# Optimization experiments

Hardware: AMD Instinct MI355X
Metric: run time of the kernel (lower is better)

The kernel has to match this reference:

```python
import jax, jax.numpy as jnp
import numpy as np

EPS = 1e-5
BOUNDARY = 1.0 - EPS
TEMP = 0.5  # temperature from init_kwargs


def _safe_sqrt(t):
    # sqrt with zero (not inf/nan) gradient at t<=0; matches the analytic clamp
    # in the original custom backward (clamp(z*beta, min=eps)).
    pos = t > 0
    return jnp.where(pos, jnp.sqrt(jnp.where(pos, t, 1.0)), 0.0)


def _poincare_sim(z):
    # z: [2N, D]. Pairwise Poincare distance computed via the matmul identity
    # ||u-v||^2 = ||u||^2 + ||v||^2 - 2 u.v instead of a (2N,2N,D) broadcast.
    raw = jnp.sum(z * z, axis=-1)                      # [2N] unclamped sq norms
    sqc = jnp.clip(raw, 0.0, BOUNDARY)                 # clamped as in forward
    sqdist = jnp.maximum(raw[:, None] + raw[None, :] - 2.0 * (z @ z.T), 0.0)
    x = sqdist / ((1.0 - sqc[:, None]) * (1.0 - sqc[None, :])) * 2.0 + 1.0
    dist = jnp.log(x + _safe_sqrt(x * x - 1.0))        # arcosh(x)
    return 1.0 / (1.0 + dist)                          # Poincare similarity


def setup_inputs() -> dict:
    key = jax.random.key(0)
    k1, k2, k3, k4 = jax.random.split(key, 4)
    N, D = 4096, 8

    def ball(kg, kr):
        g = jax.random.normal(kg, (N, D), dtype=jnp.float32)
        r = jax.random.uniform(kr, (N, 1), dtype=jnp.float32) * 0.85
        return g * r / (jnp.linalg.norm(g, axis=-1, keepdims=True) + 1e-6)

    return {"z_i": ball(k1, k2), "z_j": ball(k3, k4)}


def reference(z_i, z_j):
    N = z_i.shape[0]
    z = jnp.concatenate([z_i, z_j], axis=0)            # [2N, D]
    sim = _poincare_sim(z)                             # [2N, 2N]
    idx = jnp.arange(N)
    # diag(sim, +N) and diag(sim, -N): positive pairs
    positives = jnp.concatenate([sim[idx, idx + N], sim[idx + N, idx]])  # [2N]
    mask = 1.0 - jnp.eye(2 * N, dtype=sim.dtype)       # exclude self-similarity
    denom = jnp.sum(mask * jnp.exp(sim / TEMP), axis=1)  # [2N]
    all_losses = -(positives / TEMP - jnp.log(denom))
    return jnp.sum(all_losses) / (2 * N)
```

## Files before the change

### kernel.cpp

```cpp
#include <hip/hip_runtime.h>
#include <math.h>


#define D 8
#define QS 12
#define TWO_N 8192
#define HALF_N 4096
constexpr int BLOCK = 256;
constexpr int JC    = 32;
constexpr int NTILE = 2176;
constexpr int NSEG  = 368;
constexpr int SEG_LO = 1776;
#define BOUNDARY (1.0f - 1e-5f)
#define LN2 0.6931471805599453f

typedef float f32x2 __attribute__((ext_vector_type(2)));

__device__ __forceinline__ float frcp(float x)  { return __builtin_amdgcn_rcpf(x); }
__device__ __forceinline__ float fsqrt(float x) { return __builtin_amdgcn_sqrtf(x); }
__device__ __forceinline__ float flog2(float x) { return __builtin_amdgcn_logf(x); }
__device__ __forceinline__ f32x2 splat(float v) { return (f32x2){v, v}; }

__device__ __forceinline__ float dpp_wave_sum(float v) {
    int x;
    x = __builtin_amdgcn_update_dpp(0, __float_as_int(v), 0x111, 0xf, 0xf, false);
    v += __int_as_float(x);
    x = __builtin_amdgcn_update_dpp(0, __float_as_int(v), 0x112, 0xf, 0xf, false);
    v += __int_as_float(x);
    x = __builtin_amdgcn_update_dpp(0, __float_as_int(v), 0x114, 0xf, 0xe, false);
    v += __int_as_float(x);
    x = __builtin_amdgcn_update_dpp(0, __float_as_int(v), 0x118, 0xf, 0xc, false);
    v += __int_as_float(x);
    x = __builtin_amdgcn_update_dpp(0, __float_as_int(v), 0x142, 0xa, 0xf, false);
    v += __int_as_float(x);
    x = __builtin_amdgcn_update_dpp(0, __float_as_int(v), 0x143, 0xc, 0xf, false);
    v += __int_as_float(x);
    return v;
}

__global__ __launch_bounds__(256) void prep_kernel(
    const float* __restrict__ zi, const float* __restrict__ zj,
    float* __restrict__ q, float* __restrict__ denom, float* __restrict__ out,
    float2* __restrict__ tab)
{
    const int row = blockIdx.x * 256 + threadIdx.x;
    const float* src = (row < HALF_N) ? (zi + (size_t)row * D)
                                      : (zj + (size_t)(row - HALF_N) * D);
    float4 a = *(const float4*)(src);
    float4 b = *(const float4*)(src + 4);
    float raw = a.x*a.x + a.y*a.y + a.z*a.z + a.w*a.w
              + b.x*b.x + b.y*b.y + b.z*b.z + b.w*b.w;
    float inv = frcp(1.0f - fminf(raw, BOUNDARY));
    float* dst = q + (size_t)row * QS;
    *(float4*)(dst)     = a;
    *(float4*)(dst + 4) = b;
    *(float4*)(dst + 8) = make_float4(inv, inv * raw, 0.0f, 0.0f);
    denom[row] = 0.0f;
    if (row == 0) out[0] = 0.0f;

    if (row < NSEG) {
        const int m0 = row + SEG_LO;
        const int m1 = m0 + 1;
        float ua_f = __uint_as_float(((unsigned)(m0 >> 4) << 23) | ((unsigned)(m0 & 15) << 19));
        float ub_f = __uint_as_float(((unsigned)(m1 >> 4) << 23) | ((unsigned)(m1 & 15) << 19));
        double ua = (double)ua_f, ub = (double)ub_f;
        double ga = exp(2.0 / (1.0 + log(1.0 + ua + sqrt(ua * (ua + 2.0)))));
        double gb = exp(2.0 / (1.0 + log(1.0 + ub + sqrt(ub * (ub + 2.0)))));
        double sl = (gb - ga) / (ub - ua);
        double ic = ga - sl * ua;
        tab[row] = make_float2((float)sl, (float)ic);
    }
}

__device__ __forceinline__ f32x2 dot_col(const f32x2* __restrict__ p2,
                                         const float* __restrict__ qq)
{
    float4 a  = *(const float4*)(qq);
    float4 bb = *(const float4*)(qq + 4);
    float2 c  = *(const float2*)(qq + 8);
    f32x2 x = splat(0.0f);
    x = __builtin_elementwise_fma(p2[0], splat(a.x),  x);
    x = __builtin_elementwise_fma(p2[1], splat(a.y),  x);
    x = __builtin_elementwise_fma(p2[2], splat(a.z),  x);
    x = __builtin_elementwise_fma(p2[3], splat(a.w),  x);
    x = __builtin_elementwise_fma(p2[4], splat(bb.x), x);
    x = __builtin_elementwise_fma(p2[5], splat(bb.y), x);
    x = __builtin_elementwise_fma(p2[6], splat(bb.z), x);
    x = __builtin_elementwise_fma(p2[7], splat(bb.w), x);
    x = __builtin_elementwise_fma(p2[8], splat(c.x),  x);
    x = __builtin_elementwise_fma(p2[9], splat(c.y),  x);
    return x;
}

__device__ __forceinline__ float lut1(float u, const float2* __restrict__ tab)
{
    int t = (int)(__float_as_uint(u) >> 19) - SEG_LO;
    t = (t < 0) ? 0 : t;
    t = (t > NSEG - 1) ? NSEG - 1 : t;
    float2 si = tab[t];
    return fmaf(si.x, u, si.y);
}

__global__ __launch_bounds__(BLOCK, 8) void pair_kernel(
    const float* __restrict__ q, const float2* __restrict__ gtab,
    float* __restrict__ denom)
{
    __shared__ alignas(16) float2 stab[NSEG];
    __shared__ float sq[JC * QS];
    __shared__ float sdenom[JC];

    const int tid = threadIdx.x;

    const int t = blockIdx.x;
    int b = 0;
    #pragma unroll
    for (int k = 1; k < 16; ++k)
        b += (t >= (256 * k - 8 * k * (k - 1))) ? 1 : 0;
    const int Fb    = 256 * b - 8 * b * (b - 1);
    const int ibase = 512 * b;
    const int jbase = ibase + 32 * (t - Fb);
    const bool diag = (jbase < ibase + 512);

    if (tid < NSEG / 2)
        ((float4*)stab)[tid] = ((const float4*)gtab)[tid];
    if (tid < JC * QS / 4)
        ((float4*)sq)[tid] = ((const float4*)(q + (size_t)jbase * QS))[tid];
    if (tid < JC) sdenom[tid] = 0.0f;

    const int irow0 = ibase + tid;
    const int irow1 = ibase + tid + BLOCK;
    f32x2 p2[10];
    {
        const float* q0 = q + (size_t)irow0 * QS;
        const float* q1 = q + (size_t)irow1 * QS;
        float4 a0 = *(const float4*)(q0), b0 = *(const float4*)(q0 + 4);
        float4 c0 = *(const float4*)(q0 + 8);
        float4 a1 = *(const float4*)(q1), b1 = *(const float4*)(q1 + 4);
        float4 c1 = *(const float4*)(q1 + 8);
        float m0 = -4.0f * c0.x, m1 = -4.0f * c1.x;
        p2[0] = (f32x2){m0 * a0.x, m1 * a1.x};
        p2[1] = (f32x2){m0 * a0.y, m1 * a1.y};
        p2[2] = (f32x2){m0 * a0.z, m1 * a1.z};
        p2[3] = (f32x2){m0 * a0.w, m1 * a1.w};
        p2[4] = (f32x2){m0 * b0.x, m1 * b1.x};
        p2[5] = (f32x2){m0 * b0.y, m1 * b1.y};
        p2[6] = (f32x2){m0 * b0.z, m1 * b1.z};
        p2[7] = (f32x2){m0 * b0.w, m1 * b1.w};
        p2[8] = (f32x2){2.0f * c0.y, 2.0f * c1.y};
        p2[9] = (f32x2){2.0f * c0.x, 2.0f * c1.x};
    }
    f32x2 acc2 = splat(0.0f);
    __syncthreads();

    #pragma unroll 2
    for (int jp = 0; jp < JC / 2; ++jp) {
        const int jj0 = 2 * jp, jj1 = 2 * jp + 1;

        f32x2 u0 = dot_col(p2, sq + jj0 * QS);
        f32x2 u1 = dot_col(p2, sq + jj1 * QS);
        u0 = __builtin_elementwise_max(u0, splat(0.0f));
        u1 = __builtin_elementwise_max(u1, splat(0.0f));
        f32x2 e0 = (f32x2){lut1(u0.x, stab), lut1(u0.y, stab)};
        f32x2 e1 = (f32x2){lut1(u1.x, stab), lut1(u1.y, stab)};

        if (diag) {
            const int j0 = jbase + jj0, j1 = jbase + jj1;
            e0.x = (j0 > irow0) ? e0.x : 0.0f;
            e0.y = (j0 > irow1) ? e0.y : 0.0f;
            e1.x = (j1 > irow0) ? e1.x : 0.0f;
            e1.y = (j1 > irow1) ? e1.y : 0.0f;
        }
        acc2 += e0;
        acc2 += e1;

        float c0 = dpp_wave_sum(e0.x + e0.y);
        float c1 = dpp_wave_sum(e1.x + e1.y);
        if ((tid & 63) == 63) {
            atomicAdd(&sdenom[jj0], c0);
            atomicAdd(&sdenom[jj1], c1);
        }
    }

    __syncthreads();
    if (tid < JC) atomicAdd(&denom[jbase + tid], sdenom[tid]);
    atomicAdd(&denom[irow0], acc2.x);
    atomicAdd(&denom[irow1], acc2.y);
}

__global__ __launch_bounds__(1024) void reduce_kernel(
    const float* __restrict__ zi, const float* __restrict__ zj,
    const float* __restrict__ denom, float* __restrict__ out)
{
    __shared__ float s_red[1024];
    const int tid = threadIdx.x;
    const int i   = blockIdx.x * 1024 + tid;

    const int base = (i < HALF_N) ? i : (i - HALF_N);
    const float* pa = (i < HALF_N) ? (zi + (size_t)base * D) : (zj + (size_t)base * D);
    const float* pb = (i < HALF_N) ? (zj + (size_t)base * D) : (zi + (size_t)base * D);
    float4 a0 = *(const float4*)(pa), a1 = *(const float4*)(pa + 4);
    float4 b0 = *(const float4*)(pb), b1 = *(const float4*)(pb + 4);
    float rawa = a0.x*a0.x + a0.y*a0.y + a0.z*a0.z + a0.w*a0.w
               + a1.x*a1.x + a1.y*a1.y + a1.z*a1.z + a1.w*a1.w;
    float rawb = b0.x*b0.x + b0.y*b0.y + b0.z*b0.z + b0.w*b0.w
               + b1.x*b1.x + b1.y*b1.y + b1.z*b1.z + b1.w*b1.w;
    float dot  = a0.x*b0.x + a0.y*b0.y + a0.z*b0.z + a0.w*b0.w
               + a1.x*b1.x + a1.y*b1.y + a1.z*b1.z + a1.w*b1.w;
    float sqd  = fmaxf(rawa + rawb - 2.0f * dot, 0.0f);
    float inva = frcp(1.0f - fminf(rawa, BOUNDARY));
    float invb = frcp(1.0f - fminf(rawb, BOUNDARY));
    float x    = fmaf(2.0f * sqd, inva * invb, 1.0f);
    float t    = fmaf(x, x, -1.0f);
    float s    = fsqrt(fmaxf(t, 0.0f));
    float dist = flog2(x + s) * LN2;
    float sim  = frcp(1.0f + dist);
    float dlog = flog2(denom[i]) * LN2;
    float term = -(2.0f * sim - dlog);

    s_red[tid] = term;
    __syncthreads();
    for (int off = 512; off > 0; off >>= 1) {
        if (tid < off) s_red[tid] += s_red[tid + off];
        __syncthreads();
    }
    if (tid == 0) atomicAdd(out, s_red[0] * (1.0f / (float)TWO_N));
}

extern "C" void kernel_launch(void* const* d_in, const int* in_sizes, int n_in,
                              void* d_out, int out_size, void* d_ws, size_t ws_size,
                              hipStream_t stream) {
    const float* zi = (const float*)d_in[0];
    const float* zj = (const float*)d_in[1];

    float*  denom = (float*)d_ws;
    float*  q     = denom + TWO_N;
    float2* tab   = (float2*)(q + (size_t)TWO_N * QS);

    prep_kernel<<<TWO_N / 256, 256, 0, stream>>>(zi, zj, q, denom, (float*)d_out, tab);

    pair_kernel<<<NTILE, BLOCK, 0, stream>>>(q, tab, denom);

    reduce_kernel<<<TWO_N / 1024, 1024, 0, stream>>>(zi, zj, denom, (float*)d_out);
}
```

Before: 89.59 us.

## Replace symmetric triangle tiling with full-square tiles and per-chunk partial sums

Drops the upper-triangle tiling with per-column wave reductions and atomics, instead computing every row-column pair in a full 16x128 block grid that writes per-chunk row partials to a workspace. A mode-specialized inner loop keeps pair values symmetric, and the reduce kernel sums 128 partials per row and subtracts the self-pair term from the LUT. This removes atomics, DPP column reductions and LDS staging, but roughly doubles the pair evaluations and adds a multi-megabyte partials buffer.

```diff
diff --git a/kernel.cpp b/kernel.cpp
--- a/kernel.cpp
+++ b/kernel.cpp
@@ -6,9 +6,11 @@
 #define QS 12
 #define TWO_N 8192
 #define HALF_N 4096
-constexpr int BLOCK = 256;
-constexpr int JC    = 32;
-constexpr int NTILE = 2176;
+constexpr int BLOCK   = 256;
+constexpr int JC      = 64;
+constexpr int IBLOCKS = 16;
+constexpr int JCHUNKS = 128;
+constexpr int NBLK    = IBLOCKS * JCHUNKS;
 constexpr int NSEG  = 368;
 constexpr int SEG_LO = 1776;
 #define BOUNDARY (1.0f - 1e-5f)
@@ -40,8 +42,7 @@
 
 __global__ __launch_bounds__(256) void prep_kernel(
     const float* __restrict__ zi, const float* __restrict__ zj,
-    float* __restrict__ q, float* __restrict__ denom, float* __restrict__ out,
-    float2* __restrict__ tab)
+    float* __restrict__ q, float* __restrict__ out, float2* __restrict__ tab)
 {
     const int row = blockIdx.x * 256 + threadIdx.x;
     const float* src = (row < HALF_N) ? (zi + (size_t)row * D)
@@ -55,7 +56,6 @@
     *(float4*)(dst)     = a;
     *(float4*)(dst + 4) = b;
     *(float4*)(dst + 8) = make_float4(inv, inv * raw, 0.0f, 0.0f);
-    denom[row] = 0.0f;
     if (row == 0) out[0] = 0.0f;
 
     if (row < NSEG) {
@@ -72,26 +72,6 @@
     }
 }
 
-__device__ __forceinline__ f32x2 dot_col(const f32x2* __restrict__ p2,
-                                         const float* __restrict__ qq)
-{
-    float4 a  = *(const float4*)(qq);
-    float4 bb = *(const float4*)(qq + 4);
-    float2 c  = *(const float2*)(qq + 8);
-    f32x2 x = splat(0.0f);
-    x = __builtin_elementwise_fma(p2[0], splat(a.x),  x);
-    x = __builtin_elementwise_fma(p2[1], splat(a.y),  x);
-    x = __builtin_elementwise_fma(p2[2], splat(a.z),  x);
-    x = __builtin_elementwise_fma(p2[3], splat(a.w),  x);
-    x = __builtin_elementwise_fma(p2[4], splat(bb.x), x);
-    x = __builtin_elementwise_fma(p2[5], splat(bb.y), x);
-    x = __builtin_elementwise_fma(p2[6], splat(bb.z), x);
-    x = __builtin_elementwise_fma(p2[7], splat(bb.w), x);
-    x = __builtin_elementwise_fma(p2[8], splat(c.x),  x);
-    x = __builtin_elementwise_fma(p2[9], splat(c.y),  x);
-    return x;
-}
-
 __device__ __forceinline__ float lut1(float u, const float2* __restrict__ tab)
 {
     int t = (int)(__float_as_uint(u) >> 19) - SEG_LO;
@@ -101,99 +81,116 @@
     return fmaf(si.x, u, si.y);
 }
 
+template<int MODE>
+__device__ __forceinline__ f32x2 tile_loop(
+    const float* __restrict__ q, const float2* __restrict__ stab, int jbase,
+    const f32x2* __restrict__ s2, f32x2 t8, f32x2 t9, f32x2 m4,
+    int irow0, int irow1)
+{
+    f32x2 acc = splat(0.0f);
+    #pragma unroll 2
+    for (int cc = 0; cc < JC; ++cc) {
+        const float* qp = q + (size_t)(jbase + cc) * QS;
+        float4 za = *(const float4*)(qp);
+        float4 zb = *(const float4*)(qp + 4);
+        float2 qc = *(const float2*)(qp + 8);
+
+        f32x2 S = splat(0.0f);
+        S = __builtin_elementwise_fma(s2[0], splat(za.x), S);
+        S = __builtin_elementwise_fma(s2[1], splat(za.y), S);
+        S = __builtin_elementwise_fma(s2[2], splat(za.z), S);
+        S = __builtin_elementwise_fma(s2[3], splat(za.w), S);
+        S = __builtin_elementwise_fma(s2[4], splat(zb.x), S);
+        S = __builtin_elementwise_fma(s2[5], splat(zb.y), S);
+        S = __builtin_elementwise_fma(s2[6], splat(zb.z), S);
+        S = __builtin_elementwise_fma(s2[7], splat(zb.w), S);
+
+        f32x2 A = t8 * splat(qc.x);
+        A = __builtin_elementwise_fma(t9, splat(qc.y), A);
+
+        f32x2 msel;
+        if (MODE == 0) {
+            msel = m4;
+        } else {
+            const float nm = -4.0f * qc.x;
+            if (MODE == 1) {
+                msel = splat(nm);
+            } else {
+                const int j = jbase + cc;
+                msel.x = (j > irow0) ? m4.x : nm;
+                msel.y = (j > irow1) ? m4.y : nm;
+            }
+        }
+        f32x2 u = __builtin_elementwise_fma(S, msel, A);
+        u = __builtin_elementwise_max(u, splat(0.0f));
+        acc.x += lut1(u.x, stab);
+        acc.y += lut1(u.y, stab);
+    }
+    return acc;
+}
+
 __global__ __launch_bounds__(BLOCK, 8) void pair_kernel(
     const float* __restrict__ q, const float2* __restrict__ gtab,
-    float* __restrict__ denom)
+    float* __restrict__ part)
 {
     __shared__ alignas(16) float2 stab[NSEG];
-    __shared__ float sq[JC * QS];
-    __shared__ float sdenom[JC];
-
-    const int tid = threadIdx.x;
-
-    const int t = blockIdx.x;
-    int b = 0;
-    #pragma unroll
-    for (int k = 1; k < 16; ++k)
-        b += (t >= (256 * k - 8 * k * (k - 1))) ? 1 : 0;
-    const int Fb    = 256 * b - 8 * b * (b - 1);
-    const int ibase = 512 * b;
-    const int jbase = ibase + 32 * (t - Fb);
-    const bool diag = (jbase < ibase + 512);
+
+    const int tid   = threadIdx.x;
+    const int ib    = blockIdx.x >> 7;
+    const int jc    = blockIdx.x & (JCHUNKS - 1);
+    const int ibase = ib * 512;
+    const int jbase = jc * JC;
 
     if (tid < NSEG / 2)
         ((float4*)stab)[tid] = ((const float4*)gtab)[tid];
-    if (tid < JC * QS / 4)
-        ((float4*)sq)[tid] = ((const float4*)(q + (size_t)jbase * QS))[tid];
-    if (tid < JC) sdenom[tid] = 0.0f;
 
     const int irow0 = ibase + tid;
-    const int irow1 = ibase + tid + BLOCK;
-    f32x2 p2[10];
+    const int irow1 = irow0 + 256;
+    f32x2 s2[8], t8, t9, m4;
     {
         const float* q0 = q + (size_t)irow0 * QS;
         const float* q1 = q + (size_t)irow1 * QS;
         float4 a0 = *(const float4*)(q0), b0 = *(const float4*)(q0 + 4);
-        float4 c0 = *(const float4*)(q0 + 8);
+        float2 c0 = *(const float2*)(q0 + 8);
         float4 a1 = *(const float4*)(q1), b1 = *(const float4*)(q1 + 4);
-        float4 c1 = *(const float4*)(q1 + 8);
-        float m0 = -4.0f * c0.x, m1 = -4.0f * c1.x;
-        p2[0] = (f32x2){m0 * a0.x, m1 * a1.x};
-        p2[1] = (f32x2){m0 * a0.y, m1 * a1.y};
-        p2[2] = (f32x2){m0 * a0.z, m1 * a1.z};
-        p2[3] = (f32x2){m0 * a0.w, m1 * a1.w};
-        p2[4] = (f32x2){m0 * b0.x, m1 * b1.x};
-        p2[5] = (f32x2){m0 * b0.y, m1 * b1.y};
-        p2[6] = (f32x2){m0 * b0.z, m1 * b1.z};
-        p2[7] = (f32x2){m0 * b0.w, m1 * b1.w};
-        p2[8] = (f32x2){2.0f * c0.y, 2.0f * c1.y};
-        p2[9] = (f32x2){2.0f * c0.x, 2.0f * c1.x};
-    }
-    f32x2 acc2 = splat(0.0f);
+        float2 c1 = *(const float2*)(q1 + 8);
+        s2[0] = (f32x2){a0.x, a1.x}; s2[1] = (f32x2){a0.y, a1.y};
+        s2[2] = (f32x2){a0.z, a1.z}; s2[3] = (f32x2){a0.w, a1.w};
+        s2[4] = (f32x2){b0.x, b1.x}; s2[5] = (f32x2){b0.y, b1.y};
+        s2[6] = (f32x2){b0.z, b1.z}; s2[7] = (f32x2){b0.w, b1.w};
+        t8 = (f32x2){2.0f * c0.y, 2.0f * c1.y};
+        t9 = (f32x2){2.0f * c0.x, 2.0f * c1.x};
+        m4 = (f32x2){-4.0f * c0.x, -4.0f * c1.x};
+    }
     __syncthreads();
 
-    #pragma unroll 2
-    for (int jp = 0; jp < JC / 2; ++jp) {
-        const int jj0 = 2 * jp, jj1 = 2 * jp + 1;
-
-        f32x2 u0 = dot_col(p2, sq + jj0 * QS);
-        f32x2 u1 = dot_col(p2, sq + jj1 * QS);
-        u0 = __builtin_elementwise_max(u0, splat(0.0f));
-        u1 = __builtin_elementwise_max(u1, splat(0.0f));
-        f32x2 e0 = (f32x2){lut1(u0.x, stab), lut1(u0.y, stab)};
-        f32x2 e1 = (f32x2){lut1(u1.x, stab), lut1(u1.y, stab)};
-
-        if (diag) {
-            const int j0 = jbase + jj0, j1 = jbase + jj1;
-            e0.x = (j0 > irow0) ? e0.x : 0.0f;
-            e0.y = (j0 > irow1) ? e0.y : 0.0f;
-            e1.x = (j1 > irow0) ? e1.x : 0.0f;
-            e1.y = (j1 > irow1) ? e1.y : 0.0f;
-        }
-        acc2 += e0;
-        acc2 += e1;
-
-        float c0 = dpp_wave_sum(e0.x + e0.y);
-        float c1 = dpp_wave_sum(e1.x + e1.y);
-        if ((tid & 63) == 63) {
-            atomicAdd(&sdenom[jj0], c0);
-            atomicAdd(&sdenom[jj1], c1);
-        }
-    }
-
-    __syncthreads();
-    if (tid < JC) atomicAdd(&denom[jbase + tid], sdenom[tid]);
-    atomicAdd(&denom[irow0], acc2.x);
-    atomicAdd(&denom[irow1], acc2.y);
-}
-
-__global__ __launch_bounds__(1024) void reduce_kernel(
+    f32x2 acc;
+    if (jbase >= ibase + 512)
+        acc = tile_loop<0>(q, stab, jbase, s2, t8, t9, m4, irow0, irow1);
+    else if (jbase + JC <= ibase)
+        acc = tile_loop<1>(q, stab, jbase, s2, t8, t9, m4, irow0, irow1);
+    else
+        acc = tile_loop<2>(q, stab, jbase, s2, t8, t9, m4, irow0, irow1);
+
+    part[(size_t)jc * TWO_N + irow0] = acc.x;
+    part[(size_t)jc * TWO_N + irow1] = acc.y;
+}
+
+__global__ __launch_bounds__(256) void reduce_kernel(
     const float* __restrict__ zi, const float* __restrict__ zj,
-    const float* __restrict__ denom, float* __restrict__ out)
-{
-    __shared__ float s_red[1024];
+    const float* __restrict__ part, const float2* __restrict__ gtab,
+    float* __restrict__ out)
+{
+    __shared__ float swred[4];
     const int tid = threadIdx.x;
-    const int i   = blockIdx.x * 1024 + tid;
+    const int i   = blockIdx.x * 256 + tid;
+
+    float rs = 0.0f;
+    {
+        const float* pp = part + i;
+        #pragma unroll 8
+        for (int c = 0; c < JCHUNKS; ++c) rs += pp[(size_t)c * TWO_N];
+    }
 
     const int base = (i < HALF_N) ? i : (i - HALF_N);
     const float* pa = (i < HALF_N) ? (zi + (size_t)base * D) : (zj + (size_t)base * D);
@@ -214,16 +211,23 @@
     float s    = fsqrt(fmaxf(t, 0.0f));
     float dist = flog2(x + s) * LN2;
     float sim  = frcp(1.0f + dist);
-    float dlog = flog2(denom[i]) * LN2;
+
+    float cy = inva * rawa;
+    float A  = (2.0f * cy) * inva;
+    A = fmaf(2.0f * inva, cy, A);
+    float us = fmaxf(fmaf(rawa, -4.0f * inva, A), 0.0f);
+    float es = lut1(us, gtab);
+
+    float denomv = rs - es;
+    float dlog = flog2(denomv) * LN2;
     float term = -(2.0f * sim - dlog);
 
-    s_red[tid] = term;
+    float ws = dpp_wave_sum(term);
+    if ((tid & 63) == 63) swred[tid >> 6] = ws;
     __syncthreads();
-    for (int off = 512; off > 0; off >>= 1) {
-        if (tid < off) s_red[tid] += s_red[tid + off];
-        __syncthreads();
-    }
-    if (tid == 0) atomicAdd(out, s_red[0] * (1.0f / (float)TWO_N));
+    if (tid == 0)
+        atomicAdd(out, (swred[0] + swred[1] + swred[2] + swred[3])
+                           * (1.0f / (float)TWO_N));
 }
 
 extern "C" void kernel_launch(void* const* d_in, const int* in_sizes, int n_in,
@@ -232,13 +236,13 @@
     const float* zi = (const float*)d_in[0];
     const float* zj = (const float*)d_in[1];
 
-    float*  denom = (float*)d_ws;
-    float*  q     = denom + TWO_N;
-    float2* tab   = (float2*)(q + (size_t)TWO_N * QS);
-
-    prep_kernel<<<TWO_N / 256, 256, 0, stream>>>(zi, zj, q, denom, (float*)d_out, tab);
-
-    pair_kernel<<<NTILE, BLOCK, 0, stream>>>(q, tab, denom);
-
-    reduce_kernel<<<TWO_N / 1024, 1024, 0, stream>>>(zi, zj, denom, (float*)d_out);
-}
+    float*  q    = (float*)d_ws;
+    float2* tab  = (float2*)(q + (size_t)TWO_N * QS);
+    float*  part = (float*)(tab + NSEG);
+
+    prep_kernel<<<TWO_N / 256, 256, 0, stream>>>(zi, zj, q, (float*)d_out, tab);
+
+    pair_kernel<<<NBLK, BLOCK, 0, stream>>>(q, tab, part);
+
+    reduce_kernel<<<TWO_N / 256, 256, 0, stream>>>(zi, zj, part, tab, (float*)d_out);
+}
```

Result: no change. 90.69 us (+1.2%).
